# Kernel optimization log

Hardware: AMD Instinct MI355X
Metric: run time of the kernel (lower is better)

## Reference

```python
import jax, jax.numpy as jnp
import numpy as np

B = 8388608  # ~4096 stocks x 2048 trading days
D = 2048     # unique dates
LAMBDA_VOL = 0.85
LAMBDA_DIR = 0.15
TEMPERATURE = 5.0
EPS = 1e-6


def setup_inputs() -> dict:
    key = jax.random.key(0)
    k1, k2, k3, k4, k5 = jax.random.split(key, 5)
    return {
        "direction_logits": jax.random.normal(k1, (B, 2), dtype=jnp.float32),
        "direction_labels": jax.random.randint(k2, (B,), 0, 2, dtype=jnp.int64),
        "volatility_pred": jax.random.uniform(k3, (B,), dtype=jnp.float32),
        "volatility_target": jax.random.uniform(k4, (B,), dtype=jnp.float32),
        "dates": jax.random.randint(k5, (B,), 0, D, dtype=jnp.int64),
        "num_dates": D,
    }


def reference(direction_logits, direction_labels, volatility_pred, volatility_target, dates, num_dates):
    # ---- QLIKE volatility loss (masked mean) ----
    tgt, pred = volatility_target, volatility_pred
    vol_valid = (~jnp.isnan(tgt)) & (tgt > EPS) & (pred > EPS)
    pred_var = jnp.maximum(pred * pred, EPS)
    true_var = jnp.maximum(tgt * tgt, EPS)
    qlike = true_var / pred_var + jnp.log(pred_var)
    n_valid = jnp.sum(vol_valid)
    vol_loss = jnp.where(
        n_valid > 0,
        jnp.sum(jnp.where(vol_valid, qlike, 0.0)) / jnp.maximum(n_valid, 1).astype(qlike.dtype),
        0.0,
    )

    # ---- ListNet ranking loss via segmented softmax over dates ----
    dvalid = direction_labels >= 0
    p1 = jax.nn.softmax(direction_logits, axis=1)[:, 1]  # [B]

    # segmented stable softmax of p1 over each date group (valid entries only)
    pm = jax.ops.segment_max(jnp.where(dvalid, p1, -jnp.inf), dates, num_segments=num_dates)
    pe = jnp.where(dvalid, jnp.exp(p1 - pm[dates]), 0.0)
    pden = jax.ops.segment_sum(pe, dates, num_segments=num_dates)
    pred_dist = pe / jnp.maximum(pden[dates], 1e-30)

    # segmented softmax of temperature-scaled labels
    t = direction_labels.astype(p1.dtype) * TEMPERATURE
    tm = jax.ops.segment_max(jnp.where(dvalid, t, -jnp.inf), dates, num_segments=num_dates)
    te = jnp.where(dvalid, jnp.exp(t - tm[dates]), 0.0)
    tden = jax.ops.segment_sum(te, dates, num_segments=num_dates)
    true_dist = te / jnp.maximum(tden[dates], 1e-30)

    ce_el = jnp.where(dvalid, -true_dist * jnp.log(pred_dist + 1e-8), 0.0)
    ce_date = jax.ops.segment_sum(ce_el, dates, num_segments=num_dates)  # [D]
    counts = jax.ops.segment_sum(dvalid.astype(jnp.int32), dates, num_segments=num_dates)
    include = counts >= 2  # dates with < 2 stocks are skipped
    n_dates = jnp.sum(include)
    dir_loss = jnp.sum(jnp.where(include, ce_date, 0.0)) / jnp.maximum(n_dates, 1).astype(ce_date.dtype)

    total = LAMBDA_VOL * vol_loss + LAMBDA_DIR * dir_loss
    return total, vol_loss, dir_loss
```

## Files before the change

kernel.cpp:

```cpp
#include <hip/hip_runtime.h>

#define D_MAX 2048
#define EPSF 1e-6f
#define E5F 148.4131591f
#define BLK 512
#define GRID 1024


__global__ void initk(unsigned long long* g_pd, double* sum_q, unsigned* n_valid,
                      const int* ndp) {
    int i = blockIdx.x * blockDim.x + threadIdx.x;
    int nd = ndp[0]; if (nd > D_MAX) nd = D_MAX;
    if (i == 0) { *sum_q = 0.0; *n_valid = 0u; }
    if (i < nd) g_pd[i] = 0ULL;
}

__device__ __forceinline__ void volElem(float p, float tg, double& accq, unsigned& accn) {
    if (tg > EPSF && p > EPSF) {
        float pv = fmaxf(p * p, EPSF);
        float tv = fmaxf(tg * tg, EPSF);
        accq += (double)(__fdividef(tv, pv) + __logf(pv));
        accn++;
    }
}

__device__ __forceinline__ void volGroup(const float4& p4, const float4& t4,
                                         double& accq, unsigned& accn) {
    volElem(p4.x, t4.x, accq, accn);
    volElem(p4.y, t4.y, accq, accn);
    volElem(p4.z, t4.z, accq, accn);
    volElem(p4.w, t4.w, accq, accn);
}

__device__ __forceinline__ void dirElem(int lb, int d, float l0, float l1,
                                        unsigned long long* s_pack) {
    if (lb >= 0) {
        float p1 = __fdividef(1.0f, 1.0f + __expf(l0 - l1));
        float pe = __expf(p1);
        float w  = (lb >= 1) ? E5F * p1 : p1;
        unsigned stp_i = (unsigned)(w * 16.0f + 0.5f);
        unsigned pd_i  = (unsigned)(pe * 1024.0f + 0.5f);
        unsigned long long inc = (unsigned long long)stp_i
                               | ((unsigned long long)pd_i << 24)
                               | (1ULL << (48 + 8 * (lb >= 1)));
        atomicAdd(&s_pack[d], inc);
    }
}

__device__ __forceinline__ void dirGroup(const int4& l4, const int4& d4,
                                         const float4& ga, const float4& gb,
                                         unsigned long long* s_pack) {
    dirElem(l4.x, d4.x, ga.x, ga.y, s_pack);
    dirElem(l4.y, d4.y, ga.z, ga.w, s_pack);
    dirElem(l4.z, d4.z, gb.x, gb.y, s_pack);
    dirElem(l4.w, d4.w, gb.z, gb.w, s_pack);
}

__global__ __launch_bounds__(BLK, 8)
void fusedk(const float4* __restrict__ lg4, const int4* __restrict__ lab4,
            const float4* __restrict__ vp4, const float4* __restrict__ vt4,
            const int4* __restrict__ dt4, int B,
            unsigned long long* __restrict__ g_pd,
            double* __restrict__ sum_q, unsigned* __restrict__ n_valid,
            const int* __restrict__ ndp) {
    __shared__ unsigned long long s_pack[D_MAX];
    __shared__ double s_q[BLK / 64];
    __shared__ unsigned s_n[BLK / 64];
    int nd = ndp[0]; if (nd > D_MAX) nd = D_MAX;
    int B4 = B >> 2;

    for (int d = threadIdx.x; d < nd; d += BLK) s_pack[d] = 0ULL;
    __syncthreads();

    const int stride = GRID * BLK;
    int tid = blockIdx.x * BLK + threadIdx.x;
    double accq = 0.0;
    unsigned accn = 0u;

    for (int i = tid; i < B4; i += stride) {
        float4 pv = vp4[i], tv = vt4[i];
        int4   la = lab4[i], da = dt4[i];
        float4 ga = lg4[2 * i], gb = lg4[2 * i + 1];
        volGroup(pv, tv, accq, accn);
        dirGroup(la, da, ga, gb, s_pack);
    }
    int rem = B & 3;
    if (tid < rem) {
        int j = (B4 << 2) + tid;
        volElem(((const float*)vp4)[j], ((const float*)vt4)[j], accq, accn);
        dirElem(((const int*)lab4)[j], ((const int*)dt4)[j],
                ((const float*)lg4)[2 * j], ((const float*)lg4)[2 * j + 1], s_pack);
    }

    for (int o = 32; o > 0; o >>= 1) {
        accq += __shfl_down(accq, o);
        accn += __shfl_down(accn, o);
    }
    int lane = threadIdx.x & 63, wv = threadIdx.x >> 6;
    if (lane == 0) { s_q[wv] = accq; s_n[wv] = accn; }
    __syncthreads();
    if (threadIdx.x == 0) {
        double q = 0.0; unsigned nn = 0u;
        for (int w = 0; w < BLK / 64; w++) { q += s_q[w]; nn += s_n[w]; }
        atomicAdd(sum_q, q);
        atomicAdd(n_valid, nn);
    }

    int start = (blockIdx.x & 7) * BLK;
    if (start >= nd) start %= nd;
    for (int k = 0; k < (nd + BLK - 1) / BLK; k++) {
        int d0 = threadIdx.x + k * BLK;
        if (d0 < nd) {
            int d = d0 + start;
            if (d >= nd) d -= nd;
            unsigned long long c = s_pack[d];
            if (c) {
                unsigned stp24 = (unsigned)(c & 0xFFFFFFu);
                unsigned pd24  = (unsigned)((c >> 24) & 0xFFFFFFu);
                unsigned n0 = (unsigned)((c >> 48) & 0xFFu);
                unsigned n1 = (unsigned)(c >> 56);
                unsigned pd4  = (pd24 + 32u) >> 6;
                unsigned stp1 = (stp24 + 4u) >> 3;
                unsigned long long ginc = (unsigned long long)n0
                                        | ((unsigned long long)n1 << 12)
                                        | ((unsigned long long)pd4 << 24)
                                        | ((unsigned long long)stp1 << 42);
                atomicAdd(&g_pd[d], ginc);
            }
        }
    }
}

__global__ void finalk(const unsigned long long* __restrict__ g_pd, const int* __restrict__ ndp,
                       const double* __restrict__ sum_q, const unsigned* __restrict__ n_valid,
                       float* __restrict__ out) {
    __shared__ double s_ce[4];
    __shared__ unsigned s_c[4];
    int nd = ndp[0]; if (nd > D_MAX) nd = D_MAX;
    double ce = 0.0; unsigned cnt = 0u;
    for (int d = threadIdx.x; d < nd; d += 256) {
        unsigned long long pk = g_pd[d];
        unsigned n0 = (unsigned)(pk & 0xFFFu);
        unsigned n1 = (unsigned)((pk >> 12) & 0xFFFu);
        if (n0 + n1 >= 2u) {
            float pden = (float)((pk >> 24) & 0x3FFFFu) * (1.0f / 16.0f);
            float stp  = (float)(pk >> 42) * 0.5f;
            float td   = (float)n0 + (float)n1 * E5F;
            ce += (double)(__logf(fmaxf(pden, 1e-30f)) - stp / td);
            cnt++;
        }
    }
    for (int o = 32; o > 0; o >>= 1) { ce += __shfl_down(ce, o); cnt += __shfl_down(cnt, o); }
    int lane = threadIdx.x & 63, w = threadIdx.x >> 6;
    if (lane == 0) { s_ce[w] = ce; s_c[w] = cnt; }
    __syncthreads();
    if (threadIdx.x == 0) {
        double dce = s_ce[0] + s_ce[1] + s_ce[2] + s_ce[3];
        unsigned n = s_c[0] + s_c[1] + s_c[2] + s_c[3];
        unsigned nv = *n_valid;
        double vol = nv ? (*sum_q) / (double)nv : 0.0;
        double dir = dce / (double)(n ? n : 1u);
        out[0] = (float)(0.85 * vol + 0.15 * dir);
        out[1] = (float)vol;
        out[2] = (float)dir;
    }
}

extern "C" void kernel_launch(void* const* d_in, const int* in_sizes, int n_in,
                              void* d_out, int out_size, void* d_ws, size_t ws_size,
                              hipStream_t stream) {
    const float4* lg4 = (const float4*)d_in[0];
    const int4* lab4  = (const int4*)d_in[1];
    const float4* vp4 = (const float4*)d_in[2];
    const float4* vt4 = (const float4*)d_in[3];
    const int4* dt4   = (const int4*)d_in[4];
    const int* ndp    = (const int*)d_in[5];
    int B = in_sizes[1];
    float* out = (float*)d_out;

    char* ws = (char*)d_ws;
    double*   sum_q   = (double*)(ws + 0);
    unsigned* n_valid = (unsigned*)(ws + 8);
    unsigned long long* g_pd = (unsigned long long*)(ws + 64);

    initk<<<(D_MAX + 255) / 256, 256, 0, stream>>>(g_pd, sum_q, n_valid, ndp);
    fusedk<<<GRID, BLK, 0, stream>>>(lg4, lab4, vp4, vt4, dt4, B,
                                     g_pd, sum_q, n_valid, ndp);
    finalk<<<1, 256, 0, stream>>>(g_pd, ndp, sum_q, n_valid, out);
}
```

Baseline: 210.4 us.

## Replace per-block global atomics with partial-sum buffer and separate reduction kernel

Each block now writes its whole shared-memory date histogram to a per-block row in workspace instead of issuing global 64-bit atomics per date. A new reduction kernel sums the rows per date and computes the per-date cross-entropy directly, and a trivial final kernel combines the results. The aim is to remove contention from about two million global atomics. In exchange it writes and reads roughly 16 MB of partials and adds a kernel launch, and it falls back to the old path if the workspace is too small.

```diff
diff --git a/kernel.cpp b/kernel.cpp
--- a/kernel.cpp
+++ b/kernel.cpp
@@ -5,13 +5,15 @@
 #define E5F 148.4131591f
 #define BLK 512
 #define GRID 1024
+#define RBLK 256
+#define DATES_PER_RBLK 16
 
 
 __global__ void initk(unsigned long long* g_pd, double* sum_q, unsigned* n_valid,
-                      const int* ndp) {
+                      double* sum_ce, unsigned* n_dates, const int* ndp) {
     int i = blockIdx.x * blockDim.x + threadIdx.x;
     int nd = ndp[0]; if (nd > D_MAX) nd = D_MAX;
-    if (i == 0) { *sum_q = 0.0; *n_valid = 0u; }
+    if (i == 0) { *sum_q = 0.0; *n_valid = 0u; *sum_ce = 0.0; *n_dates = 0u; }
     if (i < nd) g_pd[i] = 0ULL;
 }
 
@@ -56,11 +58,13 @@
     dirElem(l4.w, d4.w, gb.z, gb.w, s_pack);
 }
 
+template<bool PART_PATH>
 __global__ __launch_bounds__(BLK, 8)
 void fusedk(const float4* __restrict__ lg4, const int4* __restrict__ lab4,
             const float4* __restrict__ vp4, const float4* __restrict__ vt4,
             const int4* __restrict__ dt4, int B,
             unsigned long long* __restrict__ g_pd,
+            unsigned long long* __restrict__ part,
             double* __restrict__ sum_q, unsigned* __restrict__ n_valid,
             const int* __restrict__ ndp) {
     __shared__ unsigned long long s_pack[D_MAX];
@@ -106,28 +110,93 @@
         atomicAdd(n_valid, nn);
     }
 
-    int start = (blockIdx.x & 7) * BLK;
-    if (start >= nd) start %= nd;
-    for (int k = 0; k < (nd + BLK - 1) / BLK; k++) {
-        int d0 = threadIdx.x + k * BLK;
-        if (d0 < nd) {
-            int d = d0 + start;
-            if (d >= nd) d -= nd;
-            unsigned long long c = s_pack[d];
+    if (PART_PATH) {
+        unsigned long long* row = part + (size_t)blockIdx.x * D_MAX;
+        for (int d = threadIdx.x; d < nd; d += BLK) row[d] = s_pack[d];
+    } else {
+        int start = (blockIdx.x & 7) * BLK;
+        if (start >= nd) start %= nd;
+        for (int k = 0; k < (nd + BLK - 1) / BLK; k++) {
+            int d0 = threadIdx.x + k * BLK;
+            if (d0 < nd) {
+                int d = d0 + start;
+                if (d >= nd) d -= nd;
+                unsigned long long c = s_pack[d];
+                if (c) {
+                    unsigned stp24 = (unsigned)(c & 0xFFFFFFu);
+                    unsigned pd24  = (unsigned)((c >> 24) & 0xFFFFFFu);
+                    unsigned n0 = (unsigned)((c >> 48) & 0xFFu);
+                    unsigned n1 = (unsigned)(c >> 56);
+                    unsigned pd4  = (pd24 + 32u) >> 6;
+                    unsigned stp1 = (stp24 + 4u) >> 3;
+                    unsigned long long ginc = (unsigned long long)n0
+                                            | ((unsigned long long)n1 << 12)
+                                            | ((unsigned long long)pd4 << 24)
+                                            | ((unsigned long long)stp1 << 42);
+                    atomicAdd(&g_pd[d], ginc);
+                }
+            }
+        }
+    }
+}
+
+__global__ __launch_bounds__(RBLK)
+void reducek(const unsigned long long* __restrict__ part, const int* __restrict__ ndp,
+             double* __restrict__ sum_ce, unsigned* __restrict__ n_dates) {
+    __shared__ unsigned s_n0[RBLK], s_n1[RBLK], s_pd[RBLK], s_st[RBLK];
+    int nd = ndp[0]; if (nd > D_MAX) nd = D_MAX;
+    int j = threadIdx.x & 15;
+    int r = threadIdx.x >> 4;
+    int d = blockIdx.x * DATES_PER_RBLK + j;
+    unsigned n0 = 0, n1 = 0, pd = 0, st = 0;
+    if (d < nd) {
+        #pragma unroll 4
+        for (int b = r; b < GRID; b += 16) {
+            unsigned long long c = part[(size_t)b * D_MAX + d];
             if (c) {
                 unsigned stp24 = (unsigned)(c & 0xFFFFFFu);
                 unsigned pd24  = (unsigned)((c >> 24) & 0xFFFFFFu);
-                unsigned n0 = (unsigned)((c >> 48) & 0xFFu);
-                unsigned n1 = (unsigned)(c >> 56);
-                unsigned pd4  = (pd24 + 32u) >> 6;
-                unsigned stp1 = (stp24 + 4u) >> 3;
-                unsigned long long ginc = (unsigned long long)n0
-                                        | ((unsigned long long)n1 << 12)
-                                        | ((unsigned long long)pd4 << 24)
-                                        | ((unsigned long long)stp1 << 42);
-                atomicAdd(&g_pd[d], ginc);
+                n0 += (unsigned)((c >> 48) & 0xFFu);
+                n1 += (unsigned)(c >> 56);
+                pd += (pd24 + 32u) >> 6;
+                st += (stp24 + 4u) >> 3;
             }
         }
+    }
+    s_n0[threadIdx.x] = n0; s_n1[threadIdx.x] = n1;
+    s_pd[threadIdx.x] = pd; s_st[threadIdx.x] = st;
+    __syncthreads();
+    if (threadIdx.x < DATES_PER_RBLK) {
+        int dd = blockIdx.x * DATES_PER_RBLK + threadIdx.x;
+        unsigned a0 = 0, a1 = 0, ap = 0, as = 0;
+        for (int rr = 0; rr < 16; rr++) {
+            int idx = rr * 16 + threadIdx.x;
+            a0 += s_n0[idx]; a1 += s_n1[idx]; ap += s_pd[idx]; as += s_st[idx];
+        }
+        double ce = 0.0; unsigned cnt = 0u;
+        if (dd < nd && a0 + a1 >= 2u) {
+            float pden = (float)ap * (1.0f / 16.0f);
+            float stp  = (float)as * 0.5f;
+            float td   = (float)a0 + (float)a1 * E5F;
+            ce = (double)(__logf(fmaxf(pden, 1e-30f)) - stp / td);
+            cnt = 1u;
+        }
+        for (int o = 8; o > 0; o >>= 1) { ce += __shfl_down(ce, o); cnt += __shfl_down(cnt, o); }
+        if (threadIdx.x == 0) { atomicAdd(sum_ce, ce); atomicAdd(n_dates, cnt); }
+    }
+}
+
+__global__ void finalk2(const double* __restrict__ sum_q, const unsigned* __restrict__ n_valid,
+                        const double* __restrict__ sum_ce, const unsigned* __restrict__ n_dates,
+                        float* __restrict__ out) {
+    if (threadIdx.x == 0 && blockIdx.x == 0) {
+        unsigned nv = *n_valid;
+        double vol = nv ? (*sum_q) / (double)nv : 0.0;
+        unsigned n = *n_dates;
+        double dir = (*sum_ce) / (double)(n ? n : 1u);
+        out[0] = (float)(0.85 * vol + 0.15 * dir);
+        out[1] = (float)vol;
+        out[2] = (float)dir;
     }
 }
 
@@ -181,10 +250,23 @@
     char* ws = (char*)d_ws;
     double*   sum_q   = (double*)(ws + 0);
     unsigned* n_valid = (unsigned*)(ws + 8);
+    unsigned* n_dates = (unsigned*)(ws + 12);
+    double*   sum_ce  = (double*)(ws + 16);
     unsigned long long* g_pd = (unsigned long long*)(ws + 64);
-
-    initk<<<(D_MAX + 255) / 256, 256, 0, stream>>>(g_pd, sum_q, n_valid, ndp);
-    fusedk<<<GRID, BLK, 0, stream>>>(lg4, lab4, vp4, vt4, dt4, B,
-                                     g_pd, sum_q, n_valid, ndp);
-    finalk<<<1, 256, 0, stream>>>(g_pd, ndp, sum_q, n_valid, out);
-}
+    unsigned long long* part = (unsigned long long*)(ws + 64 + D_MAX * 8);
+
+    size_t need = 64 + (size_t)D_MAX * 8 + (size_t)GRID * D_MAX * 8;
+    bool pathA = (ws_size >= need);
+
+    initk<<<(D_MAX + 255) / 256, 256, 0, stream>>>(g_pd, sum_q, n_valid, sum_ce, n_dates, ndp);
+    if (pathA) {
+        fusedk<true><<<GRID, BLK, 0, stream>>>(lg4, lab4, vp4, vt4, dt4, B,
+                                               g_pd, part, sum_q, n_valid, ndp);
+        reducek<<<D_MAX / DATES_PER_RBLK, RBLK, 0, stream>>>(part, ndp, sum_ce, n_dates);
+        finalk2<<<1, 64, 0, stream>>>(sum_q, n_valid, sum_ce, n_dates, out);
+    } else {
+        fusedk<false><<<GRID, BLK, 0, stream>>>(lg4, lab4, vp4, vt4, dt4, B,
+                                                g_pd, part, sum_q, n_valid, ndp);
+        finalk<<<1, 256, 0, stream>>>(g_pd, ndp, sum_q, n_valid, out);
+    }
+}
```

After: 230.9 us. 9.8% more time.

## Double-buffer streaming loads with inline-asm global loads and explicit vmcnt waits

Applied to the files above, without the earlier changes.

Replaces the grid-stride streaming loop with a software-pipelined, two-bank scheme. Each bank issues six dwordx4 global loads through inline asm, and s_waitcnt vmcnt(6) lets one bank's loads stay in flight while the other bank is consumed. Launch bounds drop from 8 to 6 waves per EU to make room for the extra live registers. The aim is to keep more memory requests outstanding per thread on this bandwidth-bound kernel, at the cost of lower occupancy. The hand-written asm and waitcnt ordering is also fragile, since the compiler cannot track these loads.

```diff
diff --git a/kernel.cpp b/kernel.cpp
--- a/kernel.cpp
+++ b/kernel.cpp
@@ -6,6 +6,29 @@
 #define BLK 512
 #define GRID 1024
 
+
+typedef float f4 __attribute__((ext_vector_type(4)));
+typedef int   i4 __attribute__((ext_vector_type(4)));
+
+#define GL4(dst, p) asm volatile("global_load_dwordx4 %0, %1, off" \
+                                 : "=v"(dst) : "v"((const void*)(p)))
+
+#define WAITBANK6(pv, tv, la, da, ga, gb)                        \
+    asm volatile("s_waitcnt vmcnt(6)"                            \
+                 : "+v"(pv), "+v"(tv), "+v"(la), "+v"(da), "+v"(ga), "+v"(gb))
+#define WAITBANK0(pv, tv, la, da, ga, gb)                        \
+    asm volatile("s_waitcnt vmcnt(0)"                            \
+                 : "+v"(pv), "+v"(tv), "+v"(la), "+v"(da), "+v"(ga), "+v"(gb))
+
+#define ISSUE6(pv, tv, la, da, ga, gb, i)   \
+    do { int _i = (i);                      \
+        GL4(pv, vp4 + _i);                  \
+        GL4(tv, vt4 + _i);                  \
+        GL4(la, lab4 + _i);                 \
+        GL4(da, dt4 + _i);                  \
+        GL4(ga, lg4 + 2 * _i);              \
+        GL4(gb, lg4 + 2 * _i + 1);          \
+    } while (0)
 
 __global__ void initk(unsigned long long* g_pd, double* sum_q, unsigned* n_valid,
                       const int* ndp) {
@@ -22,14 +45,6 @@
         accq += (double)(__fdividef(tv, pv) + __logf(pv));
         accn++;
     }
-}
-
-__device__ __forceinline__ void volGroup(const float4& p4, const float4& t4,
-                                         double& accq, unsigned& accn) {
-    volElem(p4.x, t4.x, accq, accn);
-    volElem(p4.y, t4.y, accq, accn);
-    volElem(p4.z, t4.z, accq, accn);
-    volElem(p4.w, t4.w, accq, accn);
 }
 
 __device__ __forceinline__ void dirElem(int lb, int d, float l0, float l1,
@@ -47,19 +62,25 @@
     }
 }
 
-__device__ __forceinline__ void dirGroup(const int4& l4, const int4& d4,
-                                         const float4& ga, const float4& gb,
+__device__ __forceinline__ void consume6(const f4& pv, const f4& tv,
+                                         const i4& la, const i4& da,
+                                         const f4& ga, const f4& gb,
+                                         double& accq, unsigned& accn,
                                          unsigned long long* s_pack) {
-    dirElem(l4.x, d4.x, ga.x, ga.y, s_pack);
-    dirElem(l4.y, d4.y, ga.z, ga.w, s_pack);
-    dirElem(l4.z, d4.z, gb.x, gb.y, s_pack);
-    dirElem(l4.w, d4.w, gb.z, gb.w, s_pack);
-}
-
-__global__ __launch_bounds__(BLK, 8)
-void fusedk(const float4* __restrict__ lg4, const int4* __restrict__ lab4,
-            const float4* __restrict__ vp4, const float4* __restrict__ vt4,
-            const int4* __restrict__ dt4, int B,
+    volElem(pv.x, tv.x, accq, accn);
+    volElem(pv.y, tv.y, accq, accn);
+    volElem(pv.z, tv.z, accq, accn);
+    volElem(pv.w, tv.w, accq, accn);
+    dirElem(la.x, da.x, ga.x, ga.y, s_pack);
+    dirElem(la.y, da.y, ga.z, ga.w, s_pack);
+    dirElem(la.z, da.z, gb.x, gb.y, s_pack);
+    dirElem(la.w, da.w, gb.z, gb.w, s_pack);
+}
+
+__global__ __launch_bounds__(BLK, 6)
+void fusedk(const f4* __restrict__ lg4, const i4* __restrict__ lab4,
+            const f4* __restrict__ vp4, const f4* __restrict__ vt4,
+            const i4* __restrict__ dt4, int B,
             unsigned long long* __restrict__ g_pd,
             double* __restrict__ sum_q, unsigned* __restrict__ n_valid,
             const int* __restrict__ ndp) {
@@ -77,12 +98,35 @@
     double accq = 0.0;
     unsigned accn = 0u;
 
-    for (int i = tid; i < B4; i += stride) {
-        float4 pv = vp4[i], tv = vt4[i];
-        int4   la = lab4[i], da = dt4[i];
-        float4 ga = lg4[2 * i], gb = lg4[2 * i + 1];
-        volGroup(pv, tv, accq, accn);
-        dirGroup(la, da, ga, gb, s_pack);
+    int n = B4 / stride;
+    int npair = n & ~1;
+    int kdone = 0;
+
+    if (npair >= 2) {
+        f4 pvA, tvA, gaA, gbA; i4 laA, daA;
+        f4 pvB, tvB, gaB, gbB; i4 laB, daB;
+        ISSUE6(pvA, tvA, laA, daA, gaA, gbA, tid);
+        ISSUE6(pvB, tvB, laB, daB, gaB, gbB, tid + stride);
+        int k = 0;
+        for (; k + 2 < npair; k += 2) {
+            WAITBANK6(pvA, tvA, laA, daA, gaA, gbA);
+            consume6(pvA, tvA, laA, daA, gaA, gbA, accq, accn, s_pack);
+            ISSUE6(pvA, tvA, laA, daA, gaA, gbA, tid + (k + 2) * stride);
+            WAITBANK6(pvB, tvB, laB, daB, gaB, gbB);
+            consume6(pvB, tvB, laB, daB, gaB, gbB, accq, accn, s_pack);
+            ISSUE6(pvB, tvB, laB, daB, gaB, gbB, tid + (k + 3) * stride);
+        }
+        WAITBANK6(pvA, tvA, laA, daA, gaA, gbA);
+        consume6(pvA, tvA, laA, daA, gaA, gbA, accq, accn, s_pack);
+        WAITBANK0(pvB, tvB, laB, daB, gaB, gbB);
+        consume6(pvB, tvB, laB, daB, gaB, gbB, accq, accn, s_pack);
+        kdone = npair;
+    }
+    for (int i = tid + kdone * stride; i < B4; i += stride) {
+        f4 pv = vp4[i], tv = vt4[i];
+        i4 la = lab4[i], da = dt4[i];
+        f4 ga = lg4[2 * i], gb = lg4[2 * i + 1];
+        consume6(pv, tv, la, da, ga, gb, accq, accn, s_pack);
     }
     int rem = B & 3;
     if (tid < rem) {
@@ -108,8 +152,8 @@
 
     int start = (blockIdx.x & 7) * BLK;
     if (start >= nd) start %= nd;
-    for (int k = 0; k < (nd + BLK - 1) / BLK; k++) {
-        int d0 = threadIdx.x + k * BLK;
+    for (int kk = 0; kk < (nd + BLK - 1) / BLK; kk++) {
+        int d0 = threadIdx.x + kk * BLK;
         if (d0 < nd) {
             int d = d0 + start;
             if (d >= nd) d -= nd;
@@ -169,12 +213,12 @@
 extern "C" void kernel_launch(void* const* d_in, const int* in_sizes, int n_in,
                               void* d_out, int out_size, void* d_ws, size_t ws_size,
                               hipStream_t stream) {
-    const float4* lg4 = (const float4*)d_in[0];
-    const int4* lab4  = (const int4*)d_in[1];
-    const float4* vp4 = (const float4*)d_in[2];
-    const float4* vt4 = (const float4*)d_in[3];
-    const int4* dt4   = (const int4*)d_in[4];
-    const int* ndp    = (const int*)d_in[5];
+    const f4* lg4 = (const f4*)d_in[0];
+    const i4* lab4 = (const i4*)d_in[1];
+    const f4* vp4 = (const f4*)d_in[2];
+    const f4* vt4 = (const f4*)d_in[3];
+    const i4* dt4 = (const i4*)d_in[4];
+    const int* ndp = (const int*)d_in[5];
     int B = in_sizes[1];
     float* out = (float*)d_out;
 
```

Result: no change. 210.0 us (-0.2%).
